# Optimization experiments

Measured on AMD Instinct MI355X. Metric: run time of the kernel, lower is better.

## Reference

```python
import jax, jax.numpy as jnp
import numpy as np

LATENT = 256
OUT_CH = 1
K = 16
HEADS = 64


def _conv1x1(x, W, b):
    # x: [B, Cin, ...spatial], W: [Cout, Cin], b: [Cout]
    y = jnp.einsum('oc,bc...->bo...', W, x)
    return y + b.reshape((1, -1) + (1,) * (y.ndim - 2))


def _batch_gather(x, idx):
    # x: [B, C, N], idx: [B, Nq, K] -> [B, C, Nq, K]
    return jax.vmap(lambda xb, ib: xb[:, ib])(x, idx)


def setup_inputs() -> dict:
    key = jax.random.key(0)
    ks = jax.random.split(key, 16)
    B, N, NQ = 2, 10000, 10000
    inp = {
        'latents': jax.random.normal(ks[0], (B, LATENT, N), jnp.float32),
        'pts': jax.random.normal(ks[1], (B, 3, N), jnp.float32),
        'pts_query': jax.random.normal(ks[2], (B, 3, NQ), jnp.float32),
        'proj_ids': jax.random.randint(ks[3], (B, NQ, K), 0, N, jnp.int64),
    }
    def lin(k, o, i):
        s = 1.0 / np.sqrt(i)
        k1, k2 = jax.random.split(k)
        return (jax.random.uniform(k1, (o, i), jnp.float32, -s, s),
                jax.random.uniform(k2, (o,), jnp.float32, -s, s))
    inp['W1'], inp['b1'] = lin(ks[4], LATENT, LATENT + 3)
    inp['W2'], inp['b2'] = lin(ks[5], LATENT, LATENT)
    inp['W3'], inp['b3'] = lin(ks[6], LATENT, LATENT)
    inp['Wq'], inp['bq'] = lin(ks[7], HEADS, LATENT)
    inp['Wv'], inp['bv'] = lin(ks[8], LATENT, LATENT)
    inp['W8'], inp['b8'] = lin(ks[9], OUT_CH, LATENT)
    return inp


def reference(latents, pts, pts_query, proj_ids,
              W1, b1, W2, b2, W3, b3, Wq, bq, Wv, bv, W8, b8):
    # gather neighbor latents and points: [B, C, Nq, K], [B, 3, Nq, K]
    x = _batch_gather(latents, proj_ids)
    npts = _batch_gather(pts, proj_ids)
    rel = pts_query[:, :, :, None] - npts          # [B, 3, Nq, K]
    x = jnp.concatenate([x, rel], axis=1)          # [B, C+3, Nq, K]
    x = jax.nn.relu(_conv1x1(x, W1, b1))
    x = jax.nn.relu(_conv1x1(x, W2, b2))
    x = jax.nn.relu(_conv1x1(x, W3, b3))
    query = _conv1x1(x, Wq, bq)                    # [B, 64, Nq, K]
    value = _conv1x1(x, Wv, bv)                    # [B, C, Nq, K]
    attention = jax.nn.softmax(query, axis=-1).mean(axis=1)  # [B, Nq, K]
    # weighted sum over K neighbors: [B, Nq, C] -> [B, C, Nq]
    x = jnp.einsum('bnk,bcnk->bcn', attention, value)
    x = _conv1x1(x, W8, b8)                        # [B, out_ch, Nq]
    return x
```

## Files before the change

kernel.cpp:

```cpp
#include <hip/hip_runtime.h>
#include <cstdint>
#include <cstddef>


#define NLAT 256
#define KNB 16
#define QB 4
#define MROWS 64
#define ROWB 528
#define MTSTR 16896

typedef float    f32x4  __attribute__((ext_vector_type(4)));
typedef float    f32x16 __attribute__((ext_vector_type(16)));
typedef _Float16 f16x8  __attribute__((ext_vector_type(8)));
typedef _Float16 f16x4  __attribute__((ext_vector_type(4)));

struct Smem {
  unsigned char buf[MROWS * ROWB];
  float Sp[4][MROWS];
  float Sv[MROWS];
  int sidx[MROWS];
  int is64;
};

__device__ __forceinline__ void layer_mfma32(
    unsigned char* __restrict__ buf, const unsigned short* __restrict__ Wp,
    const float* __restrict__ bias, int lane, int wave, bool relu)
{
  const int lm32 = lane & 31, h = lane >> 5;
  const char* bp = (const char*)buf + lm32 * 528 + h * 16;
  const char* wbase = (const char*)Wp + (wave * 64 + lm32) * 32 + h * 16;

  f32x16 acc[2][2];
#pragma unroll
  for (int i = 0; i < 2; ++i)
#pragma unroll
    for (int j = 0; j < 2; ++j) acc[i][j] = (f32x16)(0.f);

#pragma unroll
  for (int ks = 0; ks < 16; ++ks) {
    f16x8 a[2], b[2];
#pragma unroll
    for (int ct = 0; ct < 2; ++ct)
      a[ct] = *(const f16x8*)(wbase + ks * 8192 + ct * 1024);
#pragma unroll
    for (int mt = 0; mt < 2; ++mt)
      b[mt] = *(const f16x8*)(bp + mt * MTSTR + ks * 32);
#pragma unroll
    for (int ct = 0; ct < 2; ++ct)
#pragma unroll
      for (int mt = 0; mt < 2; ++mt)
        acc[ct][mt] = __builtin_amdgcn_mfma_f32_32x32x16_f16(a[ct], b[mt], acc[ct][mt], 0, 0, 0);
  }
  __syncthreads();
#pragma unroll
  for (int ct = 0; ct < 2; ++ct) {
#pragma unroll
    for (int q = 0; q < 4; ++q) {
      const int ch0 = wave * 64 + ct * 32 + q * 8 + h * 4;
      const float4 bs = *(const float4*)(bias + ch0);
      const float bb[4] = {bs.x, bs.y, bs.z, bs.w};
#pragma unroll
      for (int mt = 0; mt < 2; ++mt) {
        f16x4 v;
#pragma unroll
        for (int j = 0; j < 4; ++j) {
          float x = acc[ct][mt][q * 4 + j] + bb[j];
          if (relu) x = fmaxf(x, 0.f);
          v[j] = (_Float16)x;
        }
        *(f16x4*)((char*)buf + (mt * 32 + lm32) * 528 + ch0 * 2) = v;
      }
    }
  }
}

extern "C" __global__ __launch_bounds__(256, 4)
void interp_mfma(const float* __restrict__ pts,
                 const float* __restrict__ ptsq,
                 const void*  __restrict__ proj,
                 const unsigned short* __restrict__ L1pre,
                 const float* __restrict__ w1rT,
                 const unsigned short* __restrict__ W2p,
                 const unsigned short* __restrict__ W3p,
                 const unsigned short* __restrict__ Wqh,
                 const float* __restrict__ b2, const float* __restrict__ b3,
                 const float* __restrict__ bq,
                 const float* __restrict__ wv8, const float* __restrict__ c0p,
                 float* __restrict__ out,
                 int N, int NQ)
{
  __shared__ Smem sm;
  const int tid = threadIdx.x;
  const int bid = blockIdx.x;
  const int lane = tid & 63, wave = tid >> 6;
  const int lm = lane & 15, lk = lane >> 4;

  if (tid == 0) {
    const int* p = (const int*)proj;
    int z = 1;
    for (int i = 0; i < 64; ++i) z &= (p[2 * i + 1] == 0);
    sm.is64 = z;
  }
  __syncthreads();
  if (tid < MROWS) {
    long long g = (long long)bid * QB + (tid >> 4);
    long long base = g * KNB + (tid & 15);
    sm.sidx[tid] = sm.is64 ? (int)((const long long*)proj)[base]
                           : ((const int*)proj)[base];
  }
  __syncthreads();

  {
    const int row = tid & 63, part = tid >> 6;
    const int id = sm.sidx[row];
    const long long g = (long long)bid * QB + (row >> 4);
    const int b = (int)(g / NQ);
    const int nq = (int)(g - (long long)b * NQ);
    float rel[3];
#pragma unroll
    for (int j = 0; j < 3; ++j)
      rel[j] = ptsq[((size_t)b * 3 + j) * NQ + nq]
             - pts[((size_t)b * 3 + j) * N + id];
    const _Float16* lp = (const _Float16*)L1pre + ((size_t)b * N + id) * NLAT + part * 64;
    const float* wr0 = w1rT + part * 64;
    const float* wr1 = w1rT + 256 + part * 64;
    const float* wr2 = w1rT + 512 + part * 64;
    char* dst = (char*)sm.buf + row * 528 + part * 128;
#pragma unroll
    for (int cc = 0; cc < 8; ++cc) {
      f16x8 v = *(const f16x8*)(lp + cc * 8);
      const float4 a0 = *(const float4*)(wr0 + cc * 8), a1 = *(const float4*)(wr0 + cc * 8 + 4);
      const float4 b0 = *(const float4*)(wr1 + cc * 8), b1_ = *(const float4*)(wr1 + cc * 8 + 4);
      const float4 c0 = *(const float4*)(wr2 + cc * 8), c1 = *(const float4*)(wr2 + cc * 8 + 4);
      const float wa[8] = {a0.x, a0.y, a0.z, a0.w, a1.x, a1.y, a1.z, a1.w};
      const float wb[8] = {b0.x, b0.y, b0.z, b0.w, b1_.x, b1_.y, b1_.z, b1_.w};
      const float wc[8] = {c0.x, c0.y, c0.z, c0.w, c1.x, c1.y, c1.z, c1.w};
      f16x8 o;
#pragma unroll
      for (int e = 0; e < 8; ++e) {
        float x = (float)v[e] + rel[0] * wa[e] + rel[1] * wb[e] + rel[2] * wc[e];
        o[e] = (_Float16)fmaxf(x, 0.f);
      }
      *(f16x8*)(dst + cc * 16) = o;
    }
  }
  __syncthreads();

  layer_mfma32(sm.buf, W2p, b2, lane, wave, true);
  __syncthreads();
  layer_mfma32(sm.buf, W3p, b3, lane, wave, true);
  __syncthreads();

  const char* bp16 = (const char*)sm.buf + lm * 528 + lk * 16;
  f32x4 qacc[4];
#pragma unroll
  for (int mt = 0; mt < 4; ++mt) qacc[mt] = (f32x4){0.f, 0.f, 0.f, 0.f};
  {
    const char* wqb = (const char*)Wqh + (wave * 16 + lm) * 512 + lk * 16;
#pragma unroll
    for (int ks = 0; ks < 8; ++ks) {
      f16x8 a = *(const f16x8*)(wqb + ks * 64);
#pragma unroll
      for (int mt = 0; mt < 4; ++mt) {
        f16x8 bf = *(const f16x8*)(bp16 + mt * 8448 + ks * 64);
        qacc[mt] = __builtin_amdgcn_mfma_f32_16x16x32_f16(a, bf, qacc[mt], 0, 0, 0);
      }
    }
  }
  {
    const char* sp = (const char*)sm.buf + (wave * 16 + lm) * 528 + lk * 16;
    float sacc = 0.f;
#pragma unroll
    for (int cc = 0; cc < 8; ++cc) {
      f16x8 v = *(const f16x8*)(sp + cc * 64);
      const int k0 = cc * 32 + lk * 8;
      const float4 w0 = *(const float4*)(wv8 + k0);
      const float4 w1 = *(const float4*)(wv8 + k0 + 4);
      sacc += (float)v[0] * w0.x + (float)v[1] * w0.y
            + (float)v[2] * w0.z + (float)v[3] * w0.w;
      sacc += (float)v[4] * w1.x + (float)v[5] * w1.y
            + (float)v[6] * w1.z + (float)v[7] * w1.w;
    }
    sacc += __shfl_xor(sacc, 16);
    sacc += __shfl_xor(sacc, 32);
    if (lk == 0) sm.Sv[wave * 16 + lm] = sacc;
  }

  {
    float bqv[4];
#pragma unroll
    for (int r = 0; r < 4; ++r) bqv[r] = bq[wave * 16 + lk * 4 + r];
#pragma unroll
    for (int mt = 0; mt < 4; ++mt) {
      float sw = 0.f;
#pragma unroll
      for (int r = 0; r < 4; ++r) {
        const float qv = qacc[mt][r] + bqv[r];
        float mx = qv;
#pragma unroll
        for (int msk = 1; msk < 16; msk <<= 1) mx = fmaxf(mx, __shfl_xor(mx, msk));
        const float e = __expf(qv - mx);
        float s = e;
#pragma unroll
        for (int msk = 1; msk < 16; msk <<= 1) s += __shfl_xor(s, msk);
        sw += e / s;
      }
      sw += __shfl_xor(sw, 16);
      sw += __shfl_xor(sw, 32);
      if (lk == 0) sm.Sp[wave][mt * 16 + lm] = sw;
    }
  }
  __syncthreads();

  {
    const int m = wave * 16 + lm;
    const float a = (sm.Sp[0][m] + sm.Sp[1][m] + sm.Sp[2][m] + sm.Sp[3][m]) * (1.f / 64.f);
    float val = a * sm.Sv[m];
#pragma unroll
    for (int msk = 1; msk < 16; msk <<= 1) val += __shfl_xor(val, msk);
    if (lane == 0) out[(long long)bid * QB + wave] = val + c0p[0];
  }
}

extern "C" __global__ __launch_bounds__(256, 4)
void l1pre_k(const unsigned short* __restrict__ Lt_u,
             const float* __restrict__ latents,
             const unsigned short* __restrict__ W1p,
             const float* __restrict__ b1,
             unsigned short* __restrict__ L1pre, int N, int use_lt)
{
  __shared__ unsigned char buf[MROWS * ROWB];
  const int tid = threadIdx.x;
  const int b = blockIdx.y, n0 = blockIdx.x * 64;
  const int lane = tid & 63, wave = tid >> 6;
  const int lm32 = lane & 31, h = lane >> 5;

  {
    const int row = tid & 63, part = tid >> 6;
    const int n = n0 + row;
    char* dst = (char*)buf + row * 528 + part * 128;
    if (n < N) {
      if (use_lt) {
        const _Float16* src = (const _Float16*)Lt_u + ((size_t)b * N + n) * NLAT + part * 64;
#pragma unroll
        for (int cc = 0; cc < 8; ++cc)
          *(f16x8*)(dst + cc * 16) = *(const f16x8*)(src + cc * 8);
      } else {
        for (int cc = 0; cc < 8; ++cc) {
          f16x8 v;
#pragma unroll
          for (int e = 0; e < 8; ++e)
            v[e] = (_Float16)latents[((size_t)b * NLAT + part * 64 + cc * 8 + e) * N + n];
          *(f16x8*)(dst + cc * 16) = v;
        }
      }
    } else {
      const f16x8 z = {0, 0, 0, 0, 0, 0, 0, 0};
#pragma unroll
      for (int cc = 0; cc < 8; ++cc) *(f16x8*)(dst + cc * 16) = z;
    }
  }
  __syncthreads();

  const char* bp = (const char*)buf + lm32 * 528 + h * 16;
  const char* wbase = (const char*)W1p + (wave * 64 + lm32) * 32 + h * 16;
  f32x16 acc[2][2];
#pragma unroll
  for (int i = 0; i < 2; ++i)
#pragma unroll
    for (int j = 0; j < 2; ++j) acc[i][j] = (f32x16)(0.f);
#pragma unroll
  for (int ks = 0; ks < 16; ++ks) {
    f16x8 a[2], bb[2];
#pragma unroll
    for (int ct = 0; ct < 2; ++ct)
      a[ct] = *(const f16x8*)(wbase + ks * 8192 + ct * 1024);
#pragma unroll
    for (int mt = 0; mt < 2; ++mt)
      bb[mt] = *(const f16x8*)(bp + mt * MTSTR + ks * 32);
#pragma unroll
    for (int ct = 0; ct < 2; ++ct)
#pragma unroll
      for (int mt = 0; mt < 2; ++mt)
        acc[ct][mt] = __builtin_amdgcn_mfma_f32_32x32x16_f16(a[ct], bb[mt], acc[ct][mt], 0, 0, 0);
  }
#pragma unroll
  for (int ct = 0; ct < 2; ++ct) {
#pragma unroll
    for (int q = 0; q < 4; ++q) {
      const int ch0 = wave * 64 + ct * 32 + q * 8 + h * 4;
      const float4 bs = *(const float4*)(b1 + ch0);
      const float bb[4] = {bs.x, bs.y, bs.z, bs.w};
#pragma unroll
      for (int mt = 0; mt < 2; ++mt) {
        const int n = n0 + mt * 32 + lm32;
        if (n < N) {
          f16x4 v;
#pragma unroll
          for (int j = 0; j < 4; ++j)
            v[j] = (_Float16)(acc[ct][mt][q * 4 + j] + bb[j]);
          *(f16x4*)((char*)L1pre + (((size_t)b * N + n) * NLAT + ch0) * 2) = v;
        }
      }
    }
  }
}

extern "C" __global__ void prep_w(const float* __restrict__ W1, const float* __restrict__ W2,
                                  const float* __restrict__ W3, const float* __restrict__ Wq,
                                  const float* __restrict__ Wv, const float* __restrict__ W8,
                                  const float* __restrict__ bv, const float* __restrict__ b8,
                                  unsigned short* W1p, unsigned short* W2p,
                                  unsigned short* W3p, unsigned short* Wqh,
                                  float* w1rT, float* wv8, float* c0) {
  const int t = blockIdx.x * 256 + threadIdx.x;
  union { _Float16 h; unsigned short u; } cv;
  if (t < 65536) {
    const int ch = t >> 8, k = t & 255;
    const int dst = (k >> 4) * 4096 + ch * 16 + (k & 15);
    cv.h = (_Float16)W1[(size_t)ch * 259 + k]; W1p[dst] = cv.u;
    cv.h = (_Float16)W2[t]; W2p[dst] = cv.u;
    cv.h = (_Float16)W3[t]; W3p[dst] = cv.u;
  }
  if (t < 16384) { cv.h = (_Float16)Wq[t]; Wqh[t] = cv.u; }
  if (t < 768) {
    const int j = t >> 8, ch = t & 255;
    w1rT[t] = W1[(size_t)ch * 259 + 256 + j];
  }
  if (t < 256) {
    float s = 0.f;
    for (int o = 0; o < 256; ++o) s += Wv[(size_t)o * 256 + t] * W8[o];
    wv8[t] = s;
  }
  if (t == 0) {
    float s = 0.f;
    for (int o = 0; o < 256; ++o) s += bv[o] * W8[o];
    c0[0] = s + b8[0];
  }
}

extern "C" __global__ void transp(const float* __restrict__ latents,
                                  unsigned short* __restrict__ Lt, int N) {
  __shared__ unsigned short tile[256][68];
  const int b = blockIdx.y, n0 = blockIdx.x * 64, tid = threadIdx.x;
  const int nl = tid & 63;
  union { _Float16 h; unsigned short u; } cv;
  for (int c = tid >> 6; c < 256; c += 4) {
    const int n = n0 + nl;
    float v = (n < N) ? latents[((size_t)b * NLAT + c) * N + n] : 0.f;
    cv.h = (_Float16)v;
    tile[c][nl] = cv.u;
  }
  __syncthreads();
  const int nr = tid >> 2, cg = (tid & 3) * 64;
  const int n = n0 + nr;
  if (n < N) {
    for (int cc = 0; cc < 64; cc += 8) {
      f16x8 v;
#pragma unroll
      for (int j = 0; j < 8; ++j) {
        union { unsigned short u; _Float16 h; } bk;
        bk.u = tile[cg + cc + j][nr];
        v[j] = bk.h;
      }
      *(f16x8*)((_Float16*)Lt + ((size_t)b * N + n) * NLAT + cg + cc) = v;
    }
  }
}

extern "C" void kernel_launch(void* const* d_in, const int* in_sizes, int n_in,
                              void* d_out, int out_size, void* d_ws, size_t ws_size,
                              hipStream_t stream) {
  (void)n_in; (void)out_size;
  const float* latents = (const float*)d_in[0];
  const float* pts     = (const float*)d_in[1];
  const float* ptsq    = (const float*)d_in[2];
  const void*  proj    = d_in[3];
  const float* W1 = (const float*)d_in[4];  const float* b1 = (const float*)d_in[5];
  const float* W2 = (const float*)d_in[6];  const float* b2 = (const float*)d_in[7];
  const float* W3 = (const float*)d_in[8];  const float* b3 = (const float*)d_in[9];
  const float* Wq = (const float*)d_in[10]; const float* bq = (const float*)d_in[11];
  const float* Wv = (const float*)d_in[12]; const float* bv = (const float*)d_in[13];
  const float* W8 = (const float*)d_in[14]; const float* b8 = (const float*)d_in[15];
  float* out = (float*)d_out;

  const int B  = 2;
  const int N  = in_sizes[1] / (3 * B);
  const int NQ = in_sizes[2] / (3 * B);

  size_t off = 0;
  auto alloc = [&](size_t bytes) -> char* {
    char* p = (char*)d_ws + off;
    off += (bytes + 255) & ~(size_t)255;
    return p;
  };
  unsigned short* W1p = (unsigned short*)alloc(65536 * 2);
  unsigned short* W2p = (unsigned short*)alloc(65536 * 2);
  unsigned short* W3p = (unsigned short*)alloc(65536 * 2);
  unsigned short* Wqh = (unsigned short*)alloc(16384 * 2);
  float* w1rT = (float*)alloc(768 * 4);
  float* wv8  = (float*)alloc(256 * 4);
  float* c0   = (float*)alloc(4);
  const size_t l1_bytes = (size_t)B * N * NLAT * 2;
  unsigned short* L1pre = (unsigned short*)alloc(l1_bytes);
  unsigned short* Lt = (unsigned short*)((char*)d_ws + off);
  const int use_lt = (off + l1_bytes <= ws_size) ? 1 : 0;

  hipLaunchKernelGGL(prep_w, dim3(256), dim3(256), 0, stream,
                     W1, W2, W3, Wq, Wv, W8, bv, b8, W1p, W2p, W3p, Wqh,
                     w1rT, wv8, c0);
  if (use_lt)
    hipLaunchKernelGGL(transp, dim3((N + 63) / 64, B), dim3(256), 0, stream,
                       latents, Lt, N);
  hipLaunchKernelGGL(l1pre_k, dim3((N + 63) / 64, B), dim3(256), 0, stream,
                     Lt, latents, W1p, b1, L1pre, N, use_lt);
  const int nblocks = (B * NQ + QB - 1) / QB;
  hipLaunchKernelGGL(interp_mfma, dim3(nblocks), dim3(256), 0, stream,
                     pts, ptsq, proj, L1pre, w1rT, W2p, W3p, Wqh,
                     b2, b3, bq, wv8, c0, out, N, NQ);
}
```

Measured before the change: 210.4 us.

## Fuse latent transpose into layer-1 precompute kernel and parallelize bias reduction

Removes the separate transpose kernel that wrote an fp16 channel-last copy of latents to workspace. l1pre_k now reads the fp32 channel-major latents directly with coalesced loads across points, converts them to fp16, and stores them transposed into shared memory. This drops one launch and a full round trip of the transposed buffer through global memory. Separately, the bv·W8 bias dot product in prep_w is split across 64 threads with a shuffle reduction instead of running serially on one thread.

```diff
diff --git a/kernel.cpp b/kernel.cpp
--- a/kernel.cpp
+++ b/kernel.cpp
@@ -224,11 +224,10 @@
 }
 
 extern "C" __global__ __launch_bounds__(256, 4)
-void l1pre_k(const unsigned short* __restrict__ Lt_u,
-             const float* __restrict__ latents,
+void l1pre_k(const float* __restrict__ latents,
              const unsigned short* __restrict__ W1p,
              const float* __restrict__ b1,
-             unsigned short* __restrict__ L1pre, int N, int use_lt)
+             unsigned short* __restrict__ L1pre, int N)
 {
   __shared__ unsigned char buf[MROWS * ROWB];
   const int tid = threadIdx.x;
@@ -237,28 +236,19 @@
   const int lm32 = lane & 31, h = lane >> 5;
 
   {
-    const int row = tid & 63, part = tid >> 6;
-    const int n = n0 + row;
-    char* dst = (char*)buf + row * 528 + part * 128;
-    if (n < N) {
-      if (use_lt) {
-        const _Float16* src = (const _Float16*)Lt_u + ((size_t)b * N + n) * NLAT + part * 64;
-#pragma unroll
-        for (int cc = 0; cc < 8; ++cc)
-          *(f16x8*)(dst + cc * 16) = *(const f16x8*)(src + cc * 8);
-      } else {
-        for (int cc = 0; cc < 8; ++cc) {
-          f16x8 v;
-#pragma unroll
-          for (int e = 0; e < 8; ++e)
-            v[e] = (_Float16)latents[((size_t)b * NLAT + part * 64 + cc * 8 + e) * N + n];
-          *(f16x8*)(dst + cc * 16) = v;
-        }
-      }
-    } else {
-      const f16x8 z = {0, 0, 0, 0, 0, 0, 0, 0};
-#pragma unroll
-      for (int cc = 0; cc < 8; ++cc) *(f16x8*)(dst + cc * 16) = z;
+    const int nl = tid & 63;
+    const int n = n0 + nl;
+    const bool ok = (n < N);
+#pragma unroll
+    for (int jj = 0; jj < 8; ++jj) {
+      const int j = (tid >> 6) + jj * 4;
+      f16x8 v;
+#pragma unroll
+      for (int e = 0; e < 8; ++e) {
+        const float x = ok ? latents[((size_t)b * NLAT + j * 8 + e) * N + n] : 0.f;
+        v[e] = (_Float16)x;
+      }
+      *(f16x8*)((char*)buf + nl * 528 + j * 16) = v;
     }
   }
   __syncthreads();
@@ -333,46 +323,20 @@
     for (int o = 0; o < 256; ++o) s += Wv[(size_t)o * 256 + t] * W8[o];
     wv8[t] = s;
   }
-  if (t == 0) {
+  if (t < 64) {
     float s = 0.f;
-    for (int o = 0; o < 256; ++o) s += bv[o] * W8[o];
-    c0[0] = s + b8[0];
-  }
-}
-
-extern "C" __global__ void transp(const float* __restrict__ latents,
-                                  unsigned short* __restrict__ Lt, int N) {
-  __shared__ unsigned short tile[256][68];
-  const int b = blockIdx.y, n0 = blockIdx.x * 64, tid = threadIdx.x;
-  const int nl = tid & 63;
-  union { _Float16 h; unsigned short u; } cv;
-  for (int c = tid >> 6; c < 256; c += 4) {
-    const int n = n0 + nl;
-    float v = (n < N) ? latents[((size_t)b * NLAT + c) * N + n] : 0.f;
-    cv.h = (_Float16)v;
-    tile[c][nl] = cv.u;
-  }
-  __syncthreads();
-  const int nr = tid >> 2, cg = (tid & 3) * 64;
-  const int n = n0 + nr;
-  if (n < N) {
-    for (int cc = 0; cc < 64; cc += 8) {
-      f16x8 v;
-#pragma unroll
-      for (int j = 0; j < 8; ++j) {
-        union { unsigned short u; _Float16 h; } bk;
-        bk.u = tile[cg + cc + j][nr];
-        v[j] = bk.h;
-      }
-      *(f16x8*)((_Float16*)Lt + ((size_t)b * N + n) * NLAT + cg + cc) = v;
-    }
+#pragma unroll
+    for (int i = 0; i < 4; ++i) s += bv[t + 64 * i] * W8[t + 64 * i];
+#pragma unroll
+    for (int msk = 1; msk < 64; msk <<= 1) s += __shfl_xor(s, msk);
+    if (t == 0) c0[0] = s + b8[0];
   }
 }
 
 extern "C" void kernel_launch(void* const* d_in, const int* in_sizes, int n_in,
                               void* d_out, int out_size, void* d_ws, size_t ws_size,
                               hipStream_t stream) {
-  (void)n_in; (void)out_size;
+  (void)n_in; (void)out_size; (void)ws_size;
   const float* latents = (const float*)d_in[0];
   const float* pts     = (const float*)d_in[1];
   const float* ptsq    = (const float*)d_in[2];
@@ -402,19 +366,13 @@
   float* w1rT = (float*)alloc(768 * 4);
   float* wv8  = (float*)alloc(256 * 4);
   float* c0   = (float*)alloc(4);
-  const size_t l1_bytes = (size_t)B * N * NLAT * 2;
-  unsigned short* L1pre = (unsigned short*)alloc(l1_bytes);
-  unsigned short* Lt = (unsigned short*)((char*)d_ws + off);
-  const int use_lt = (off + l1_bytes <= ws_size) ? 1 : 0;
+  unsigned short* L1pre = (unsigned short*)alloc((size_t)B * N * NLAT * 2);
 
   hipLaunchKernelGGL(prep_w, dim3(256), dim3(256), 0, stream,
                      W1, W2, W3, Wq, Wv, W8, bv, b8, W1p, W2p, W3p, Wqh,
                      w1rT, wv8, c0);
-  if (use_lt)
-    hipLaunchKernelGGL(transp, dim3((N + 63) / 64, B), dim3(256), 0, stream,
-                       latents, Lt, N);
   hipLaunchKernelGGL(l1pre_k, dim3((N + 63) / 64, B), dim3(256), 0, stream,
-                     Lt, latents, W1p, b1, L1pre, N, use_lt);
+                     latents, W1p, b1, L1pre, N);
   const int nblocks = (B * NQ + QB - 1) / QB;
   hipLaunchKernelGGL(interp_mfma, dim3(nblocks), dim3(256), 0, stream,
                      pts, ptsq, proj, L1pre, w1rT, W2p, W3p, Wqh,
```

After: 198.2 us. -5.8%, faster.
